# Optimization experiments

Measured on AMD Instinct MI355X. Metric: run time of the kernel, lower is better.

## Reference

```python
import jax, jax.numpy as jnp
import numpy as np

# Faithful JAX port of RayObsGraph.forward with T=1.
# torch_geometric GraphConv(x, edge_index) with add-aggregation and no edge
# weights computes: out[i] = lin_root(x[i]) + lin_rel(sum_{(j->i) in E} x[j]),
# where lin_root has no bias and lin_rel has a bias. dense_to_sparse(adj)
# yields an edge (row j -> col i) for every nonzero adj[j, i], so the
# aggregation equals binarize(adj)^T @ x, computed batched here instead of the
# original per-sample Python loop.

GS = 128      # graph_size
OBS = 1024    # obs_dim
H = 256       # gcn_h_size
OUT = 1024    # gcn_outsize
NO = 18       # num_outputs
B = 256

def setup_inputs() -> dict:
    key = jax.random.key(0)
    ks = jax.random.split(key, 16)
    inp = {
        "flat": jax.random.normal(ks[0], (B, OBS), jnp.float32),
        "nodes": jax.random.normal(ks[1], (B, GS, OBS), jnp.float32),
        "num_nodes": jax.random.randint(ks[2], (B,), 0, GS),
        "adj": jax.random.randint(ks[3], (B, GS, GS), 0, 2),
        "seq_lens": jnp.ones((B,), jnp.int32),
        # GraphConv 0: lin_rel (bias) + lin_root (no bias)
        "W0_rel": jax.random.normal(ks[4], (OBS, H), jnp.float32) / np.sqrt(OBS),
        "b0": jnp.zeros((H,), jnp.float32),
        "W0_root": jax.random.normal(ks[5], (OBS, H), jnp.float32) / np.sqrt(OBS),
        # GraphConv 1
        "W1_rel": jax.random.normal(ks[6], (H, OUT), jnp.float32) / np.sqrt(H),
        "b1": jnp.zeros((OUT,), jnp.float32),
        "W1_root": jax.random.normal(ks[7], (H, OUT), jnp.float32) / np.sqrt(H),
        # logit / value branches (SlimFC, activation None)
        "Wl": jax.random.normal(ks[8], (OUT, NO), jnp.float32) / np.sqrt(OUT),
        "bl": jnp.zeros((NO,), jnp.float32),
        "Wv": jax.random.normal(ks[9], (OUT, 1), jnp.float32) / np.sqrt(OUT),
        "bv": jnp.zeros((1,), jnp.float32),
    }
    return inp

def _forward(flat, nodes, adj, num_nodes,
             W0_rel, b0, W0_root, W1_rel, b1, W1_root, Wl, bl, Wv, bv):
    bsz = flat.shape[0]
    bi = jnp.arange(bsz)
    n = num_nodes
    nm1 = jnp.maximum(n - 1, 0)
    has_prev = n > 0

    # dense_to_sparse treats any nonzero entry as an edge (weight unused)
    A = (adj != 0).astype(flat.dtype)                       # [B, GS, GS]
    A = A.at[bi, n, n].set(1.0)
    A = A.at[bi, n, nm1].set(jnp.where(has_prev, 1.0, A[bi, n, nm1]))
    A = A.at[bi, nm1, n].set(jnp.where(has_prev, 1.0, A[bi, nm1, n]))

    # write current observation into node slot num_nodes
    x = nodes.at[bi, n].set(flat)                           # [B, GS, OBS]

    At = jnp.swapaxes(A, 1, 2)                              # message j->i: A^T
    aggr0 = jnp.einsum('bij,bjd->bid', At, x)               # [B, GS, OBS]
    h0 = jax.nn.relu(aggr0 @ W0_rel + b0 + x @ W0_root)     # [B, GS, H]
    aggr1 = jnp.einsum('bij,bjd->bid', At, h0)              # [B, GS, H]
    h1 = jax.nn.relu(aggr1 @ W1_rel + b1 + h0 @ W1_root)    # [B, GS, OUT]

    node_out = h1[bi, n]                                    # [B, OUT]
    logits = node_out @ Wl + bl                             # [B, NO]
    values = (node_out @ Wv + bv).squeeze(-1)               # [B]
    return logits, values

def reference(flat, nodes, num_nodes, adj, seq_lens,
              W0_rel, b0, W0_root, W1_rel, b1, W1_root, Wl, bl, Wv, bv):
    # seq_lens only determines B = len(seq_lens); T = flat.shape[0] // B = 1
    del seq_lens
    return _forward(flat, nodes, adj, num_nodes,
                    W0_rel, b0, W0_root, W1_rel, b1, W1_root, Wl, bl, Wv, bv)
```

## Files before the change

kernel.cpp:

```cpp
#include <hip/hip_runtime.h>
#include <hip/hip_bf16.h>
#include <cstdint>
#include <cstddef>

#define GS     128
#define OBS    1024
#define HSZ    256
#define OUTSZ  1024
#define NOUT   18
#define BATCH  256

typedef short  short8  __attribute__((ext_vector_type(8)));
typedef float  f32x4   __attribute__((ext_vector_type(4)));

__device__ __forceinline__ uint32_t f2bf_bits(float f) {
  uint32_t u = __builtin_bit_cast(uint32_t, f);
  return (u + 0x7fffu + ((u >> 16) & 1u)) >> 16;
}
__device__ __forceinline__ float bf_bits2f(uint32_t b) {
  return __builtin_bit_cast(float, b << 16);
}
__device__ __forceinline__ uint4 cvt8s(const float4 a, const float4 b) {
  float v[8] = {a.x, a.y, a.z, a.w, b.x, b.y, b.z, b.w};
  uint32_t h[8];
#pragma unroll
  for (int e = 0; e < 8; ++e) h[e] = f2bf_bits(v[e]);
  return make_uint4(h[0] | (h[1] << 16), h[2] | (h[3] << 16),
                    h[4] | (h[5] << 16), h[6] | (h[7] << 16));
}

__global__ __launch_bounds__(256) void prep_kernel(
    const float* __restrict__ W0_rel, const float* __restrict__ W0_root,
    ushort* __restrict__ WtP, const float* __restrict__ Wl,
    const float* __restrict__ Wv, float* __restrict__ WlT,
    const float* __restrict__ W1_rel, const float* __restrict__ W1_root,
    ushort* __restrict__ W1bf)
{
  __shared__ float T[64][65];
  const int blk = blockIdx.x;
  const int t = threadIdx.x;
  if (blk < 128) {
    const int k0 = (blk & 15) * 64;
    const int n0 = (blk >> 4) * 64;
    for (int idx = t; idx < 4096; idx += 256) {
      const int r = idx >> 6, c = idx & 63;
      const int n = n0 + c;
      T[r][c] = (n < HSZ) ? W0_rel[(size_t)(k0 + r) * HSZ + n]
                          : W0_root[(size_t)(k0 + r) * HSZ + (n - HSZ)];
    }
    __syncthreads();
    for (int idx = t; idx < 4096; idx += 256) {
      const int r = idx >> 6, c = idx & 63;
      const int kk = k0 + c;
      WtP[((size_t)((kk >> 5) * 512 + n0 + r)) * 32 + (kk & 31)] =
          (ushort)f2bf_bits(T[c][r]);
    }
  } else if (blk < 132) {
    const int o = (blk - 128) * 256 + t;
#pragma unroll
    for (int c = 0; c < NOUT; ++c)
      WlT[(size_t)c * OUTSZ + o] = Wl[(size_t)o * NOUT + c];
    WlT[(size_t)18 * OUTSZ + o] = Wv[o];
  } else {
    const int base = (blk - 132) * 16384;
    for (int it = 0; it < 64; ++it) {
      const int idx = base + it * 256 + t;
      const int k = idx >> 10, o = idx & 1023;
      const float v = (k < HSZ) ? W1_rel[(size_t)k * OUTSZ + o]
                                : W1_root[(size_t)(k - HSZ) * OUTSZ + o];
      W1bf[idx] = (ushort)f2bf_bits(v);
    }
  }
}

__global__ __launch_bounds__(256, 2) void gemm0_mfma(
    const float* __restrict__ flat, const float* __restrict__ nodes,
    const int* __restrict__ num_nodes, const ushort* __restrict__ WtP,
    ushort* __restrict__ YT)
{
  __shared__ ushort As[64][40];

  const int mh = blockIdx.x;
  const int b  = blockIdx.y;
  const int nb = num_nodes[b];
  const int t  = threadIdx.x;

  const int arow = t >> 2;
  const int akb  = (t & 3) * 8;
  const int g = mh * 64 + arow;
  const float* xsrc = ((g == nb) ? (flat + (size_t)b * OBS)
                                 : (nodes + ((size_t)b * GS + g) * OBS)) + akb;

  const int wv = t >> 6;
  const int lane = t & 63;
  const int ln = lane & 15, q = lane >> 4;

  const ushort* bptr = WtP + ((size_t)(wv * 128 + ln)) * 32 + q * 8;

  f32x4 acc[8][4] = {};

  float4 pa0 = *(const float4*)(xsrc);
  float4 pa1 = *(const float4*)(xsrc + 4);
  float4 qa0, qa1;

  short8 bha[8], bhb[8];
#pragma unroll
  for (int jj = 0; jj < 8; ++jj)
    bha[jj] = *(const short8*)(bptr + jj * 512);

  for (int ks = 0; ks < 32; ks += 2) {
    *(uint4*)&As[arow][akb] = cvt8s(pa0, pa1);
    __syncthreads();
    {
      const int kn = ks + 1;
      qa0 = *(const float4*)(xsrc + kn * 32);
      qa1 = *(const float4*)(xsrc + kn * 32 + 4);
      const ushort* bp = bptr + (size_t)kn * 16384;
#pragma unroll
      for (int jj = 0; jj < 8; ++jj)
        bhb[jj] = *(const short8*)(bp + jj * 512);
    }
    short8 ah[4];
#pragma unroll
    for (int ii = 0; ii < 4; ++ii)
      ah[ii] = *(const short8*)&As[ii * 16 + ln][q * 8];
#pragma unroll
    for (int jj = 0; jj < 8; ++jj)
#pragma unroll
      for (int ii = 0; ii < 4; ++ii)
        acc[jj][ii] = __builtin_amdgcn_mfma_f32_16x16x32_bf16(
            bha[jj], ah[ii], acc[jj][ii], 0, 0, 0);
    __syncthreads();

    *(uint4*)&As[arow][akb] = cvt8s(qa0, qa1);
    __syncthreads();
    if (ks + 2 < 32) {
      const int kn = ks + 2;
      pa0 = *(const float4*)(xsrc + kn * 32);
      pa1 = *(const float4*)(xsrc + kn * 32 + 4);
      const ushort* bp = bptr + (size_t)kn * 16384;
#pragma unroll
      for (int jj = 0; jj < 8; ++jj)
        bha[jj] = *(const short8*)(bp + jj * 512);
    }
#pragma unroll
    for (int ii = 0; ii < 4; ++ii)
      ah[ii] = *(const short8*)&As[ii * 16 + ln][q * 8];
#pragma unroll
    for (int jj = 0; jj < 8; ++jj)
#pragma unroll
      for (int ii = 0; ii < 4; ++ii)
        acc[jj][ii] = __builtin_amdgcn_mfma_f32_16x16x32_bf16(
            bhb[jj], ah[ii], acc[jj][ii], 0, 0, 0);
    __syncthreads();
  }

#pragma unroll
  for (int jj = 0; jj < 8; ++jj) {
    const int hp = wv * 128 + jj * 16 + q * 4;
    const int kofs = (hp < 256) ? 0 : 128;
#pragma unroll
    for (int ii = 0; ii < 4; ++ii) {
      const int kidx = kofs + mh * 64 + ii * 16 + ln;
#pragma unroll
      for (int r = 0; r < 4; ++r) {
        const int h2 = (hp + r) & 255;
        YT[((size_t)b * 256 + h2) * 256 + kidx] =
            (ushort)f2bf_bits(acc[jj][ii][r]);
      }
    }
  }
}

__global__ __launch_bounds__(256, 2) void fused_aggr(
    const ushort* __restrict__ YT, const int* __restrict__ adj,
    const int* __restrict__ num_nodes, const float* __restrict__ b0,
    float* __restrict__ Z)
{
  __shared__ ushort   Ys[128][264];
  __shared__ uint32_t rm[128][4];
  __shared__ uint32_t cmL[128][4];

  const int hh = blockIdx.x;
  const int b  = blockIdx.y;
  const int n  = num_nodes[b];
  const int t  = threadIdx.x;
  const int wv = t >> 6, lane = t & 63;
  const int ln = lane & 15, q = lane >> 4;

  for (int it = 0; it < 16; ++it) {
    const int id = t + it * 256;
    const int row = id >> 5, c8 = (id & 31) * 8;
    *(uint4*)&Ys[row][c8] =
        *(const uint4*)&YT[((size_t)(b * 256 + hh * 128 + row)) * 256 + c8];
  }

#pragma unroll 4
  for (int i = 0; i < 32; ++i) {
    const int k = wv * 32 + i;
    const int* arow = adj + ((size_t)b * GS + k) * GS;
    const unsigned long long m0 = __ballot(arow[lane] != 0);
    const unsigned long long m1 = __ballot(arow[64 + lane] != 0);
    if (lane == 0) {
      rm[k][0] = (uint32_t)m0; rm[k][1] = (uint32_t)(m0 >> 32);
      rm[k][2] = (uint32_t)m1; rm[k][3] = (uint32_t)(m1 >> 32);
    }
  }
  __syncthreads();
  if (t < 128) {
    uint32_t c0 = 0, c1 = 0, c2 = 0, c3 = 0;
    const int w = t >> 5, sh = t & 31;
#pragma unroll 8
    for (int k = 0; k < 128; ++k) {
      const uint32_t bit = (rm[k][w] >> sh) & 1u;
      if (k < 32)      c0 |= bit << k;
      else if (k < 64) c1 |= bit << (k - 32);
      else if (k < 96) c2 |= bit << (k - 64);
      else             c3 |= bit << (k - 96);
    }
    cmL[t][0] = c0; cmL[t][1] = c1; cmL[t][2] = c2; cmL[t][3] = c3;
  }
  __syncthreads();
  if (t == 0) {
    cmL[n][n >> 5] |= 1u << (n & 31);
    if (n > 0) {
      cmL[n - 1][n >> 5] |= 1u << (n & 31);
      cmL[n][(n - 1) >> 5] |= 1u << ((n - 1) & 31);
    }
  }
  __syncthreads();

  f32x4 acc[8][2] = {};
  for (int ks = 0; ks < 4; ++ks) {
    short8 bf[2];
#pragma unroll
    for (int ht = 0; ht < 2; ++ht)
      bf[ht] = *(const short8*)&Ys[wv * 32 + ht * 16 + ln][ks * 32 + q * 8];
#pragma unroll
    for (int jt = 0; jt < 8; ++jt) {
      const uint32_t w = cmL[jt * 16 + ln][ks];
      const uint32_t byte = (w >> (q * 8)) & 0xFFu;
      short8 af;
#pragma unroll
      for (int i = 0; i < 8; ++i)
        af[i] = (short)(((byte >> i) & 1u) ? 0x3F80 : 0);
#pragma unroll
      for (int ht = 0; ht < 2; ++ht)
        acc[jt][ht] = __builtin_amdgcn_mfma_f32_16x16x32_bf16(
            af, bf[ht], acc[jt][ht], 0, 0, 0);
    }
  }

  const uint32_t S0 = cmL[n][0], S1 = cmL[n][1], S2 = cmL[n][2], S3 = cmL[n][3];
  float bb[2];
#pragma unroll
  for (int ht = 0; ht < 2; ++ht) bb[ht] = b0[hh * 128 + wv * 32 + ht * 16 + ln];

  float asum[2] = {0.f, 0.f};
#pragma unroll
  for (int jt = 0; jt < 8; ++jt)
#pragma unroll
    for (int r = 0; r < 4; ++r) {
      const int j = jt * 16 + q * 4 + r;
      const uint32_t Sw = (j < 32) ? S0 : (j < 64) ? S1 : (j < 96) ? S2 : S3;
      const bool sj = (Sw >> (j & 31)) & 1u;
      const bool isn = (j == n);
#pragma unroll
      for (int ht = 0; ht < 2; ++ht) {
        const int hl = wv * 32 + ht * 16 + ln;
        const float yroot = bf_bits2f(Ys[hl][128 + j]);
        const float v = fmaxf(bb[ht] + yroot + acc[jt][ht][r], 0.f);
        if (sj) asum[ht] += v;
        if (isn) Z[(size_t)b * 512 + 256 + hh * 128 + hl] = v;
      }
    }

#pragma unroll
  for (int ht = 0; ht < 2; ++ht) {
    float s = asum[ht];
    s += __shfl_down(s, 32);
    s += __shfl_down(s, 16);
    if (ln == lane)
      Z[(size_t)b * 512 + hh * 128 + wv * 32 + ht * 16 + ln] = s;
  }
}

__global__ __launch_bounds__(256) void gemm1_head(
    const float* __restrict__ Z, const ushort* __restrict__ W1bf,
    const float* __restrict__ b1, const float* __restrict__ WlT,
    const float* __restrict__ bl, const float* __restrict__ bv,
    float* __restrict__ out)
{
  __shared__ float Zl[512];
  __shared__ float pl[19][4];

  const int b = blockIdx.x;
  const int t = threadIdx.x;
  const int wv = t >> 6, lane = t & 63;
  const int o4 = t * 4;

  Zl[t]       = Z[(size_t)b * 512 + t];
  Zl[256 + t] = Z[(size_t)b * 512 + 256 + t];
  __syncthreads();

  float4 a = *(const float4*)&b1[o4];
  const ushort* wp = W1bf + o4;
#pragma unroll 8
  for (int k = 0; k < 512; ++k) {
    const ushort4 w4 = *(const ushort4*)(wp + (size_t)k * OUTSZ);
    const float s = Zl[k];
    a.x = fmaf(s, bf_bits2f(w4.x), a.x);
    a.y = fmaf(s, bf_bits2f(w4.y), a.y);
    a.z = fmaf(s, bf_bits2f(w4.z), a.z);
    a.w = fmaf(s, bf_bits2f(w4.w), a.w);
  }
  a.x = fmaxf(a.x, 0.f); a.y = fmaxf(a.y, 0.f);
  a.z = fmaxf(a.z, 0.f); a.w = fmaxf(a.w, 0.f);

  float p[19];
#pragma unroll
  for (int c = 0; c < 19; ++c) {
    const float4 w = *(const float4*)&WlT[(size_t)c * OUTSZ + o4];
    p[c] = a.x * w.x + a.y * w.y + a.z * w.z + a.w * w.w;
  }
#pragma unroll
  for (int c = 0; c < 19; ++c) {
    float v = p[c];
    v += __shfl_down(v, 32); v += __shfl_down(v, 16);
    v += __shfl_down(v, 8);  v += __shfl_down(v, 4);
    v += __shfl_down(v, 2);  v += __shfl_down(v, 1);
    if (lane == 0) pl[c][wv] = v;
  }
  __syncthreads();
  if (t < 19) {
    const float s = pl[t][0] + pl[t][1] + pl[t][2] + pl[t][3];
    if (t < NOUT) out[(size_t)b * NOUT + t] = s + bl[t];
    else          out[(size_t)BATCH * NOUT + b] = s + bv[0];
  }
}

extern "C" void kernel_launch(void* const* d_in, const int* in_sizes, int n_in,
                              void* d_out, int out_size, void* d_ws, size_t ws_size,
                              hipStream_t stream)
{
  const float* flat      = (const float*)d_in[0];
  const float* nodes     = (const float*)d_in[1];
  const int*   num_nodes = (const int*)  d_in[2];
  const int*   adj       = (const int*)  d_in[3];
  const float* W0_rel    = (const float*)d_in[5];
  const float* b0        = (const float*)d_in[6];
  const float* W0_root   = (const float*)d_in[7];
  const float* W1_rel    = (const float*)d_in[8];
  const float* b1        = (const float*)d_in[9];
  const float* W1_root   = (const float*)d_in[10];
  const float* Wl        = (const float*)d_in[11];
  const float* bl        = (const float*)d_in[12];
  const float* Wv        = (const float*)d_in[13];
  const float* bv        = (const float*)d_in[14];
  float* out = (float*)d_out;

  char* ws = (char*)d_ws;
  ushort* YT   = (ushort*)ws;  ws += (size_t)BATCH * 256 * 256 * 2;
  ushort* WtP  = (ushort*)ws;  ws += (size_t)512 * OBS * 2;
  float*  WlT  = (float*)ws;   ws += (size_t)19 * OUTSZ * 4;
  ushort* W1bf = (ushort*)ws;  ws += (size_t)512 * OUTSZ * 2;
  float*  Z    = (float*)ws;   ws += (size_t)BATCH * 512 * 4;

  prep_kernel<<<164, 256, 0, stream>>>(
      W0_rel, W0_root, WtP, Wl, Wv, WlT, W1_rel, W1_root, W1bf);
  gemm0_mfma<<<dim3(2, BATCH), 256, 0, stream>>>(
      flat, nodes, num_nodes, WtP, YT);
  fused_aggr<<<dim3(2, BATCH), 256, 0, stream>>>(YT, adj, num_nodes, b0, Z);
  gemm1_head<<<BATCH, 256, 0, stream>>>(Z, W1bf, b1, WlT, bl, bv, out);
}
```

Measured before the change: 335.6 us.

## Fuse gemm0, aggregation and head into one per-sample mega kernel

Merges the three per-batch kernels into a single kernel with one block per sample. The GEMM0 result stays in shared memory, so the YT and Z workspace round trips to global memory and two launches go away. In exchange, the grid shrinks from 512 blocks to 256 with occupancy 1 and a 64-accumulator tile per thread. This raises register pressure, and there may be too few blocks to fill 256 CUs with any latency hiding.

After: 318.3 us. -5.2%, faster.

```diff
diff --git a/kernel.cpp b/kernel.cpp
--- a/kernel.cpp
+++ b/kernel.cpp
@@ -73,127 +73,27 @@
   }
 }
 
-__global__ __launch_bounds__(256, 2) void gemm0_mfma(
+__global__ __launch_bounds__(256, 1) void mega_kernel(
     const float* __restrict__ flat, const float* __restrict__ nodes,
-    const int* __restrict__ num_nodes, const ushort* __restrict__ WtP,
-    ushort* __restrict__ YT)
+    const int* __restrict__ num_nodes, const int* __restrict__ adj,
+    const float* __restrict__ b0, const ushort* __restrict__ WtP,
+    const ushort* __restrict__ W1bf, const float* __restrict__ b1,
+    const float* __restrict__ WlT, const float* __restrict__ bl,
+    const float* __restrict__ bv, float* __restrict__ out)
 {
-  __shared__ ushort As[64][40];
-
-  const int mh = blockIdx.x;
-  const int b  = blockIdx.y;
-  const int nb = num_nodes[b];
-  const int t  = threadIdx.x;
-
-  const int arow = t >> 2;
-  const int akb  = (t & 3) * 8;
-  const int g = mh * 64 + arow;
-  const float* xsrc = ((g == nb) ? (flat + (size_t)b * OBS)
-                                 : (nodes + ((size_t)b * GS + g) * OBS)) + akb;
-
-  const int wv = t >> 6;
-  const int lane = t & 63;
-  const int ln = lane & 15, q = lane >> 4;
-
-  const ushort* bptr = WtP + ((size_t)(wv * 128 + ln)) * 32 + q * 8;
-
-  f32x4 acc[8][4] = {};
-
-  float4 pa0 = *(const float4*)(xsrc);
-  float4 pa1 = *(const float4*)(xsrc + 4);
-  float4 qa0, qa1;
-
-  short8 bha[8], bhb[8];
-#pragma unroll
-  for (int jj = 0; jj < 8; ++jj)
-    bha[jj] = *(const short8*)(bptr + jj * 512);
-
-  for (int ks = 0; ks < 32; ks += 2) {
-    *(uint4*)&As[arow][akb] = cvt8s(pa0, pa1);
-    __syncthreads();
-    {
-      const int kn = ks + 1;
-      qa0 = *(const float4*)(xsrc + kn * 32);
-      qa1 = *(const float4*)(xsrc + kn * 32 + 4);
-      const ushort* bp = bptr + (size_t)kn * 16384;
-#pragma unroll
-      for (int jj = 0; jj < 8; ++jj)
-        bhb[jj] = *(const short8*)(bp + jj * 512);
-    }
-    short8 ah[4];
-#pragma unroll
-    for (int ii = 0; ii < 4; ++ii)
-      ah[ii] = *(const short8*)&As[ii * 16 + ln][q * 8];
-#pragma unroll
-    for (int jj = 0; jj < 8; ++jj)
-#pragma unroll
-      for (int ii = 0; ii < 4; ++ii)
-        acc[jj][ii] = __builtin_amdgcn_mfma_f32_16x16x32_bf16(
-            bha[jj], ah[ii], acc[jj][ii], 0, 0, 0);
-    __syncthreads();
-
-    *(uint4*)&As[arow][akb] = cvt8s(qa0, qa1);
-    __syncthreads();
-    if (ks + 2 < 32) {
-      const int kn = ks + 2;
-      pa0 = *(const float4*)(xsrc + kn * 32);
-      pa1 = *(const float4*)(xsrc + kn * 32 + 4);
-      const ushort* bp = bptr + (size_t)kn * 16384;
-#pragma unroll
-      for (int jj = 0; jj < 8; ++jj)
-        bha[jj] = *(const short8*)(bp + jj * 512);
-    }
-#pragma unroll
-    for (int ii = 0; ii < 4; ++ii)
-      ah[ii] = *(const short8*)&As[ii * 16 + ln][q * 8];
-#pragma unroll
-    for (int jj = 0; jj < 8; ++jj)
-#pragma unroll
-      for (int ii = 0; ii < 4; ++ii)
-        acc[jj][ii] = __builtin_amdgcn_mfma_f32_16x16x32_bf16(
-            bhb[jj], ah[ii], acc[jj][ii], 0, 0, 0);
-    __syncthreads();
-  }
-
-#pragma unroll
-  for (int jj = 0; jj < 8; ++jj) {
-    const int hp = wv * 128 + jj * 16 + q * 4;
-    const int kofs = (hp < 256) ? 0 : 128;
-#pragma unroll
-    for (int ii = 0; ii < 4; ++ii) {
-      const int kidx = kofs + mh * 64 + ii * 16 + ln;
-#pragma unroll
-      for (int r = 0; r < 4; ++r) {
-        const int h2 = (hp + r) & 255;
-        YT[((size_t)b * 256 + h2) * 256 + kidx] =
-            (ushort)f2bf_bits(acc[jj][ii][r]);
-      }
-    }
-  }
-}
-
-__global__ __launch_bounds__(256, 2) void fused_aggr(
-    const ushort* __restrict__ YT, const int* __restrict__ adj,
-    const int* __restrict__ num_nodes, const float* __restrict__ b0,
-    float* __restrict__ Z)
-{
-  __shared__ ushort   Ys[128][264];
+  __shared__ ushort   Ys[256][264];
+  __shared__ ushort   As[128][40];
   __shared__ uint32_t rm[128][4];
   __shared__ uint32_t cmL[128][4];
-
-  const int hh = blockIdx.x;
-  const int b  = blockIdx.y;
-  const int n  = num_nodes[b];
+  __shared__ float    a1s[256];
+  __shared__ float    rns[256];
+  __shared__ float    pl[19][4];
+
+  const int b  = blockIdx.x;
+  const int nb = num_nodes[b];
   const int t  = threadIdx.x;
   const int wv = t >> 6, lane = t & 63;
   const int ln = lane & 15, q = lane >> 4;
-
-  for (int it = 0; it < 16; ++it) {
-    const int id = t + it * 256;
-    const int row = id >> 5, c8 = (id & 31) * 8;
-    *(uint4*)&Ys[row][c8] =
-        *(const uint4*)&YT[((size_t)(b * 256 + hh * 128 + row)) * 256 + c8];
-  }
 
 #pragma unroll 4
   for (int i = 0; i < 32; ++i) {
@@ -222,20 +122,110 @@
   }
   __syncthreads();
   if (t == 0) {
-    cmL[n][n >> 5] |= 1u << (n & 31);
-    if (n > 0) {
-      cmL[n - 1][n >> 5] |= 1u << (n & 31);
-      cmL[n][(n - 1) >> 5] |= 1u << ((n - 1) & 31);
-    }
-  }
-  __syncthreads();
-
-  f32x4 acc[8][2] = {};
+    cmL[nb][nb >> 5] |= 1u << (nb & 31);
+    if (nb > 0) {
+      cmL[nb - 1][nb >> 5] |= 1u << (nb & 31);
+      cmL[nb][(nb - 1) >> 5] |= 1u << ((nb - 1) & 31);
+    }
+  }
+
+  const int arow2 = t >> 1;
+  const int akb   = (t & 1) * 16;
+  const float* xsrc = ((arow2 == nb) ? (flat + (size_t)b * OBS)
+                                     : (nodes + ((size_t)b * GS + arow2) * OBS)) + akb;
+  const ushort* bptr = WtP + ((size_t)(wv * 128 + ln)) * 32 + q * 8;
+
+  f32x4 acc[8][8] = {};
+
+  float4 pa0 = *(const float4*)(xsrc);
+  float4 pa1 = *(const float4*)(xsrc + 4);
+  float4 pa2 = *(const float4*)(xsrc + 8);
+  float4 pa3 = *(const float4*)(xsrc + 12);
+  float4 qa0, qa1, qa2, qa3;
+
+  short8 bha[8], bhb[8];
+#pragma unroll
+  for (int jj = 0; jj < 8; ++jj)
+    bha[jj] = *(const short8*)(bptr + jj * 512);
+
+  for (int ks = 0; ks < 32; ks += 2) {
+    *(uint4*)&As[arow2][akb]     = cvt8s(pa0, pa1);
+    *(uint4*)&As[arow2][akb + 8] = cvt8s(pa2, pa3);
+    {
+      const int kn = (ks + 1) * 32;
+      qa0 = *(const float4*)(xsrc + kn);
+      qa1 = *(const float4*)(xsrc + kn + 4);
+      qa2 = *(const float4*)(xsrc + kn + 8);
+      qa3 = *(const float4*)(xsrc + kn + 12);
+    }
+    __syncthreads();
+    {
+      const ushort* bp = bptr + (size_t)(ks + 1) * 16384;
+#pragma unroll
+      for (int jj = 0; jj < 8; ++jj)
+        bhb[jj] = *(const short8*)(bp + jj * 512);
+    }
+    short8 ah[8];
+#pragma unroll
+    for (int ii = 0; ii < 8; ++ii)
+      ah[ii] = *(const short8*)&As[ii * 16 + ln][q * 8];
+#pragma unroll
+    for (int jj = 0; jj < 8; ++jj)
+#pragma unroll
+      for (int ii = 0; ii < 8; ++ii)
+        acc[jj][ii] = __builtin_amdgcn_mfma_f32_16x16x32_bf16(
+            bha[jj], ah[ii], acc[jj][ii], 0, 0, 0);
+    __syncthreads();
+
+    *(uint4*)&As[arow2][akb]     = cvt8s(qa0, qa1);
+    *(uint4*)&As[arow2][akb + 8] = cvt8s(qa2, qa3);
+    if (ks + 2 < 32) {
+      const int kn = (ks + 2) * 32;
+      pa0 = *(const float4*)(xsrc + kn);
+      pa1 = *(const float4*)(xsrc + kn + 4);
+      pa2 = *(const float4*)(xsrc + kn + 8);
+      pa3 = *(const float4*)(xsrc + kn + 12);
+    }
+    __syncthreads();
+    if (ks + 2 < 32) {
+      const ushort* bp = bptr + (size_t)(ks + 2) * 16384;
+#pragma unroll
+      for (int jj = 0; jj < 8; ++jj)
+        bha[jj] = *(const short8*)(bp + jj * 512);
+    }
+#pragma unroll
+    for (int ii = 0; ii < 8; ++ii)
+      ah[ii] = *(const short8*)&As[ii * 16 + ln][q * 8];
+#pragma unroll
+    for (int jj = 0; jj < 8; ++jj)
+#pragma unroll
+      for (int ii = 0; ii < 8; ++ii)
+        acc[jj][ii] = __builtin_amdgcn_mfma_f32_16x16x32_bf16(
+            bhb[jj], ah[ii], acc[jj][ii], 0, 0, 0);
+    __syncthreads();
+  }
+
+#pragma unroll
+  for (int jj = 0; jj < 8; ++jj) {
+    const int cat = wv * 128 + jj * 16 + q * 4;
+    const int h   = cat & 255;
+    const int kof = (cat < 256) ? 0 : 128;
+#pragma unroll
+    for (int ii = 0; ii < 8; ++ii) {
+      const int kk = kof + ii * 16 + ln;
+#pragma unroll
+      for (int r = 0; r < 4; ++r)
+        Ys[h + r][kk] = (ushort)f2bf_bits(acc[jj][ii][r]);
+    }
+  }
+  __syncthreads();
+
+  f32x4 acc2[8][4] = {};
   for (int ks = 0; ks < 4; ++ks) {
-    short8 bf[2];
-#pragma unroll
-    for (int ht = 0; ht < 2; ++ht)
-      bf[ht] = *(const short8*)&Ys[wv * 32 + ht * 16 + ln][ks * 32 + q * 8];
+    short8 bf[4];
+#pragma unroll
+    for (int ht = 0; ht < 4; ++ht)
+      bf[ht] = *(const short8*)&Ys[wv * 64 + ht * 16 + ln][ks * 32 + q * 8];
 #pragma unroll
     for (int jt = 0; jt < 8; ++jt) {
       const uint32_t w = cmL[jt * 16 + ln][ks];
@@ -245,18 +235,19 @@
       for (int i = 0; i < 8; ++i)
         af[i] = (short)(((byte >> i) & 1u) ? 0x3F80 : 0);
 #pragma unroll
-      for (int ht = 0; ht < 2; ++ht)
-        acc[jt][ht] = __builtin_amdgcn_mfma_f32_16x16x32_bf16(
-            af, bf[ht], acc[jt][ht], 0, 0, 0);
-    }
-  }
-
-  const uint32_t S0 = cmL[n][0], S1 = cmL[n][1], S2 = cmL[n][2], S3 = cmL[n][3];
-  float bb[2];
-#pragma unroll
-  for (int ht = 0; ht < 2; ++ht) bb[ht] = b0[hh * 128 + wv * 32 + ht * 16 + ln];
-
-  float asum[2] = {0.f, 0.f};
+      for (int ht = 0; ht < 4; ++ht)
+        acc2[jt][ht] = __builtin_amdgcn_mfma_f32_16x16x32_bf16(
+            af, bf[ht], acc2[jt][ht], 0, 0, 0);
+    }
+  }
+
+  const uint32_t S0 = cmL[nb][0], S1 = cmL[nb][1],
+                 S2 = cmL[nb][2], S3 = cmL[nb][3];
+  float bb[4];
+#pragma unroll
+  for (int ht = 0; ht < 4; ++ht) bb[ht] = b0[wv * 64 + ht * 16 + ln];
+
+  float asum[4] = {0.f, 0.f, 0.f, 0.f};
 #pragma unroll
   for (int jt = 0; jt < 8; ++jt)
 #pragma unroll
@@ -264,51 +255,41 @@
       const int j = jt * 16 + q * 4 + r;
       const uint32_t Sw = (j < 32) ? S0 : (j < 64) ? S1 : (j < 96) ? S2 : S3;
       const bool sj = (Sw >> (j & 31)) & 1u;
-      const bool isn = (j == n);
-#pragma unroll
-      for (int ht = 0; ht < 2; ++ht) {
-        const int hl = wv * 32 + ht * 16 + ln;
+      const bool isn = (j == nb);
+#pragma unroll
+      for (int ht = 0; ht < 4; ++ht) {
+        const int hl = wv * 64 + ht * 16 + ln;
         const float yroot = bf_bits2f(Ys[hl][128 + j]);
-        const float v = fmaxf(bb[ht] + yroot + acc[jt][ht][r], 0.f);
+        const float v = fmaxf(bb[ht] + yroot + acc2[jt][ht][r], 0.f);
         if (sj) asum[ht] += v;
-        if (isn) Z[(size_t)b * 512 + 256 + hh * 128 + hl] = v;
+        if (isn) rns[hl] = v;
       }
     }
-
-#pragma unroll
-  for (int ht = 0; ht < 2; ++ht) {
+#pragma unroll
+  for (int ht = 0; ht < 4; ++ht) {
     float s = asum[ht];
     s += __shfl_down(s, 32);
     s += __shfl_down(s, 16);
-    if (ln == lane)
-      Z[(size_t)b * 512 + hh * 128 + wv * 32 + ht * 16 + ln] = s;
-  }
-}
-
-__global__ __launch_bounds__(256) void gemm1_head(
-    const float* __restrict__ Z, const ushort* __restrict__ W1bf,
-    const float* __restrict__ b1, const float* __restrict__ WlT,
-    const float* __restrict__ bl, const float* __restrict__ bv,
-    float* __restrict__ out)
-{
-  __shared__ float Zl[512];
-  __shared__ float pl[19][4];
-
-  const int b = blockIdx.x;
-  const int t = threadIdx.x;
-  const int wv = t >> 6, lane = t & 63;
+    if (q == 0) a1s[wv * 64 + ht * 16 + ln] = s;
+  }
+  __syncthreads();
+
   const int o4 = t * 4;
-
-  Zl[t]       = Z[(size_t)b * 512 + t];
-  Zl[256 + t] = Z[(size_t)b * 512 + 256 + t];
-  __syncthreads();
-
   float4 a = *(const float4*)&b1[o4];
   const ushort* wp = W1bf + o4;
 #pragma unroll 8
-  for (int k = 0; k < 512; ++k) {
+  for (int k = 0; k < 256; ++k) {
     const ushort4 w4 = *(const ushort4*)(wp + (size_t)k * OUTSZ);
-    const float s = Zl[k];
+    const float s = a1s[k];
+    a.x = fmaf(s, bf_bits2f(w4.x), a.x);
+    a.y = fmaf(s, bf_bits2f(w4.y), a.y);
+    a.z = fmaf(s, bf_bits2f(w4.z), a.z);
+    a.w = fmaf(s, bf_bits2f(w4.w), a.w);
+  }
+#pragma unroll 8
+  for (int k = 0; k < 256; ++k) {
+    const ushort4 w4 = *(const ushort4*)(wp + (size_t)(256 + k) * OUTSZ);
+    const float s = rns[k];
     a.x = fmaf(s, bf_bits2f(w4.x), a.x);
     a.y = fmaf(s, bf_bits2f(w4.y), a.y);
     a.z = fmaf(s, bf_bits2f(w4.z), a.z);
@@ -360,16 +341,12 @@
   float* out = (float*)d_out;
 
   char* ws = (char*)d_ws;
-  ushort* YT   = (ushort*)ws;  ws += (size_t)BATCH * 256 * 256 * 2;
   ushort* WtP  = (ushort*)ws;  ws += (size_t)512 * OBS * 2;
   float*  WlT  = (float*)ws;   ws += (size_t)19 * OUTSZ * 4;
   ushort* W1bf = (ushort*)ws;  ws += (size_t)512 * OUTSZ * 2;
-  float*  Z    = (float*)ws;   ws += (size_t)BATCH * 512 * 4;
 
   prep_kernel<<<164, 256, 0, stream>>>(
       W0_rel, W0_root, WtP, Wl, Wv, WlT, W1_rel, W1_root, W1bf);
-  gemm0_mfma<<<dim3(2, BATCH), 256, 0, stream>>>(
-      flat, nodes, num_nodes, WtP, YT);
-  fused_aggr<<<dim3(2, BATCH), 256, 0, stream>>>(YT, adj, num_nodes, b0, Z);
-  gemm1_head<<<BATCH, 256, 0, stream>>>(Z, W1bf, b1, WlT, bl, bv, out);
-}
+  mega_kernel<<<BATCH, 256, 0, stream>>>(
+      flat, nodes, num_nodes, adj, b0, WtP, W1bf, b1, WlT, bl, bv, out);
+}
```
